# Performance work log

Measured on AMD Instinct MI355X. Metric: run time of the kernel, lower is better.

The kernel has to match this reference:

```python
import jax, jax.numpy as jnp
import numpy as np

N, E, G = 25600, 409600, 128   # nodes, edges, graphs
IN, H, C = 200, 4, 64          # raw feat dim, heads, hidden_channels
IN2 = 2 * IN                   # after NaN-mask concat
BN_EPS = 1e-5

def _glorot(key, shape):
    lim = float(np.sqrt(6.0 / (shape[0] + shape[-1])))
    return jax.random.uniform(key, shape, jnp.float32, -lim, lim)

def setup_inputs():
    key = jax.random.key(0)
    k = iter(jax.random.split(key, 40))
    inp = {
        "x": jax.random.normal(next(k), (N, IN), jnp.float32),
        "edge_index": jax.random.randint(next(k), (2, E), 0, N, jnp.int32),
        "edge_attr": jax.random.normal(next(k), (E, 1), jnp.float32),
        "batch": jnp.repeat(jnp.arange(G, dtype=jnp.int32), N // G),
    }
    dims = [(IN2, H, C), (H * C, H, C), (H * C, 1, C)]
    for i, (din, h, c) in enumerate(dims):
        inp[f"W{i}"] = _glorot(next(k), (din, h * c))
        inp[f"as{i}"] = _glorot(next(k), (h, c))
        inp[f"ad{i}"] = _glorot(next(k), (h, c))
        inp[f"We{i}"] = _glorot(next(k), (1, h * c))
        inp[f"ae{i}"] = _glorot(next(k), (h, c))
        inp[f"b{i}"] = jnp.zeros((h * c,), jnp.float32)
    inp["bn_g"] = jnp.ones((H * C,), jnp.float32)
    inp["bn_b"] = jnp.zeros((H * C,), jnp.float32)
    inp["bn_m"] = jnp.zeros((H * C,), jnp.float32)
    inp["bn_v"] = jnp.ones((H * C,), jnp.float32)
    inp["cw1"] = _glorot(next(k), (C, C))
    inp["cb1"] = jnp.zeros((C,), jnp.float32)
    inp["cw2"] = _glorot(next(k), (C, 2))
    inp["cb2"] = jnp.zeros((2,), jnp.float32)
    return inp

def _gat(x, src, dst, ea, W, att_s, att_d, We, att_e, b, heads, ch):
    """PyG GATConv (edge_dim=1, add_self_loops=True, fill_value='mean', concat=True)."""
    n = x.shape[0]
    # self-loop edge_attr = mean of incoming edge_attr per destination node
    cnt = jax.ops.segment_sum(jnp.ones((ea.shape[0], 1), ea.dtype), dst, n)
    loop_ea = jax.ops.segment_sum(ea, dst, n) / jnp.maximum(cnt, 1.0)
    idx = jnp.arange(n, dtype=src.dtype)
    src = jnp.concatenate([src, idx])
    dst = jnp.concatenate([dst, idx])
    ea = jnp.concatenate([ea, loop_ea], axis=0)
    h = (x @ W).reshape(n, heads, ch)                      # [N,H,C]
    a_s = jnp.einsum('nhc,hc->nh', h, att_s)
    a_d = jnp.einsum('nhc,hc->nh', h, att_d)
    a_e = jnp.einsum('ehc,hc->eh', (ea @ We).reshape(-1, heads, ch), att_e)
    alpha = jax.nn.leaky_relu(a_s[src] + a_d[dst] + a_e, 0.2)   # [E',H]
    # segment softmax over destination neighborhoods
    m = jax.ops.segment_max(alpha, dst, n)
    ex = jnp.exp(alpha - m[dst])
    z = jax.ops.segment_sum(ex, dst, n)
    alpha = ex / (z[dst] + 1e-16)
    out = jax.ops.segment_sum(h[src] * alpha[:, :, None], dst, n)  # [N,H,C]
    return out.reshape(n, heads * ch) + b

def reference(x, edge_index, edge_attr, batch,
              W0, as0, ad0, We0, ae0, b0,
              W1, as1, ad1, We1, ae1, b1,
              W2, as2, ad2, We2, ae2, b2,
              bn_g, bn_b, bn_m, bn_v, cw1, cb1, cw2, cb2):
    nan_mask = jnp.isnan(x).astype(x.dtype)
    x = jnp.concatenate([jnp.nan_to_num(x), nan_mask], axis=-1)   # [N, 2*IN]
    edge_attr = jnp.nan_to_num(edge_attr)
    src, dst = edge_index[0], edge_index[1]
    for (W, a_s, a_d, We, a_e, b) in [(W0, as0, ad0, We0, ae0, b0),
                                      (W1, as1, ad1, We1, ae1, b1)]:
        x = _gat(x, src, dst, edge_attr, W, a_s, a_d, We, a_e, b, H, C)
        x = (x - bn_m) / jnp.sqrt(bn_v + BN_EPS) * bn_g + bn_b    # eval-mode BN
        x = jax.nn.relu(x)                                        # dropout = identity (eval)
    x = _gat(x, src, dst, edge_attr, W2, as2, ad2, We2, ae2, b2, 1, C)
    # global mean pool over graphs
    cnt = jax.ops.segment_sum(jnp.ones((x.shape[0], 1), x.dtype), batch, G)
    g = jax.ops.segment_sum(x, batch, G) / jnp.maximum(cnt, 1.0)  # [G, C]
    hdn = jax.nn.gelu(g @ cw1 + cb1, approximate=False)
    return hdn @ cw2 + cb2                                        # [G, 2]
```

## Files before the change

kernel.cpp:

```cpp
#include <hip/hip_runtime.h>
#include <hip/hip_bf16.h>

static const int kN  = 25600;
static const int kE  = 409600;
static const int kG  = 128;
static const int kNPG = 200;
static const int kIN = 200;
static const int kIN2 = 400;
#define BN_EPS_ 1e-5f

typedef __attribute__((ext_vector_type(8))) short short8;
typedef __attribute__((ext_vector_type(4))) float f32x4;

__device__ __forceinline__ float bu(ushort u) {
  union { float f; unsigned u32; } x; x.u32 = ((unsigned)u) << 16; return x.f;
}
__device__ __forceinline__ ushort f2u(float v) {
  __hip_bfloat16 t = __float2bfloat16(v);
  return *(ushort*)&t;
}
__device__ __forceinline__ float wredSum(float v) {
#pragma unroll
  for (int off = 1; off < 64; off <<= 1) v += __shfl_xor(v, off, 64);
  return v;
}
__device__ __forceinline__ float lrelu(float a) { return (a > 0.f) ? a : 0.2f * a; }

__global__ void k_pre(const float* __restrict__ x, ushort* __restrict__ x2,
                      int* __restrict__ deg,
                      const float* __restrict__ W0, ushort* __restrict__ Wt0,
                      const float* __restrict__ W1, ushort* __restrict__ Wt1,
                      const float* __restrict__ W2, ushort* __restrict__ Wt2,
                      const float* __restrict__ We0, const float* __restrict__ ae0,
                      const float* __restrict__ We1, const float* __restrict__ ae1,
                      const float* __restrict__ We2, const float* __restrict__ ae2,
                      float* __restrict__ wed) {
  int b = blockIdx.x, tid = threadIdx.x;
  if (b < 100) {
    deg[b * 256 + tid] = 0;
    return;
  }
  if (b < 20100) {
    int i = (b - 100) * 256 + tid;
    int n = i / kIN, j = i - n * kIN;
    float v = x[i];
    bool bad = (v != v);
    x2[(size_t)n * kIN2 + j] = f2u(bad ? 0.f : v);
    x2[(size_t)n * kIN2 + kIN + j] = f2u(bad ? 1.f : 0.f);
    return;
  }
  int pb = b - 20100;
  if (pb >= 720) {
    int l = pb - 720;
    const float* We = (l == 0) ? We0 : (l == 1) ? We1 : We2;
    const float* ae = (l == 0) ? ae0 : (l == 1) ? ae1 : ae2;
    int n = (l == 2) ? 64 : 256;
    float v = (tid < n) ? We[tid] * ae[tid] : 0.f;
    v = wredSum(v);
    if ((tid & 63) == 0 && tid < n) wed[l * 4 + (tid >> 6)] = v;
    return;
  }
  int i = pb * 256 + tid;
  if (i < 102400) {
    int n = i / kIN2, k = i - n * kIN2;
    Wt0[(size_t)n * kIN2 + k] = f2u(W0[(size_t)k * 256 + n]);
  } else if (i < 102400 + 65536) {
    int j = i - 102400;
    int n = j >> 8, k = j & 255;
    Wt1[(size_t)n * 256 + k] = f2u(W1[(size_t)k * 256 + n]);
  } else {
    int j = i - 102400 - 65536;
    int n = j >> 8, k = j & 255;
    Wt2[(size_t)n * 256 + k] = f2u(W2[(size_t)k * 64 + n]);
  }
}

#define GBK 64
#define GPAD 72

__global__ __launch_bounds__(256) void k_cnt_gemm0(
    const ushort* __restrict__ A, const ushort* __restrict__ Bt,
    ushort* __restrict__ C, const float* __restrict__ as_g,
    const float* __restrict__ ad_g, float* __restrict__ a_sg,
    float* __restrict__ a_dg, int K,
    const int* __restrict__ ei, int* __restrict__ deg, int* __restrict__ epos) {
  __shared__ ushort As[32 * GPAD];
  __shared__ ushort Bs[256 * GPAD];
  int tid = threadIdx.x;
  if (blockIdx.x >= 800) {
    int e = (blockIdx.x - 800) * 256 + tid;
    if (e < kE) epos[e] = atomicAdd(&deg[ei[kE + e]], 1);
    return;
  }
  int lane = tid & 63, w = tid >> 6;
  int l15 = lane & 15, l4 = lane >> 4;
  int row0 = blockIdx.x * 32;
  f32x4 acc[2][4] = {};
  int ach = tid & 7, arow = tid >> 3;

  for (int kt = 0; kt < K; kt += GBK) {
    __syncthreads();
    {
      int kg = kt + ach * 8;
      short8 v = {0, 0, 0, 0, 0, 0, 0, 0};
      if (kg < K) v = *(const short8*)&A[(size_t)(row0 + arow) * K + kg];
      *(short8*)&As[arow * GPAD + ach * 8] = v;
    }
#pragma unroll
    for (int p = 0; p < 8; p++) {
      int r = p * 32 + arow;
      int kg = kt + ach * 8;
      short8 v = {0, 0, 0, 0, 0, 0, 0, 0};
      if (kg < K) v = *(const short8*)&Bt[(size_t)r * K + kg];
      *(short8*)&Bs[r * GPAD + ach * 8] = v;
    }
    __syncthreads();
#pragma unroll
    for (int kk = 0; kk < 2; kk++) {
      short8 af[2], bf[4];
#pragma unroll
      for (int mi = 0; mi < 2; mi++)
        af[mi] = *(const short8*)&As[(mi * 16 + l15) * GPAD + kk * 32 + l4 * 8];
#pragma unroll
      for (int ni = 0; ni < 4; ni++)
        bf[ni] = *(const short8*)&Bs[(w * 64 + ni * 16 + l15) * GPAD + kk * 32 + l4 * 8];
#pragma unroll
      for (int mi = 0; mi < 2; mi++)
#pragma unroll
        for (int ni = 0; ni < 4; ni++)
          acc[mi][ni] = __builtin_amdgcn_mfma_f32_16x16x32_bf16(af[mi], bf[ni],
                                                                acc[mi][ni], 0, 0, 0);
    }
  }
#pragma unroll
  for (int mi = 0; mi < 2; mi++) {
    int rbase = row0 + mi * 16 + l4 * 4;
#pragma unroll
    for (int ni = 0; ni < 4; ni++) {
      int col = w * 64 + ni * 16 + l15;
#pragma unroll
      for (int r = 0; r < 4; r++)
        C[(size_t)(rbase + r) * 256 + col] = f2u(acc[mi][ni][r]);
    }
  }
  float asv[4], adv[4];
#pragma unroll
  for (int ni = 0; ni < 4; ni++) {
    asv[ni] = as_g[w * 64 + ni * 16 + l15];
    adv[ni] = ad_g[w * 64 + ni * 16 + l15];
  }
#pragma unroll
  for (int mi = 0; mi < 2; mi++) {
#pragma unroll
    for (int r = 0; r < 4; r++) {
      float ps = 0.f, pd = 0.f;
#pragma unroll
      for (int ni = 0; ni < 4; ni++) {
        ps += acc[mi][ni][r] * asv[ni];
        pd += acc[mi][ni][r] * adv[ni];
      }
#pragma unroll
      for (int off = 1; off < 16; off <<= 1) {
        ps += __shfl_xor(ps, off, 64);
        pd += __shfl_xor(pd, off, 64);
      }
      if (l15 == 0) {
        int row = row0 + mi * 16 + l4 * 4 + r;
        a_sg[row * 4 + w] = ps;
        a_dg[row * 4 + w] = pd;
      }
    }
  }
}

__global__ void k_scan_all(const int* __restrict__ deg, int* __restrict__ rowp) {
  __shared__ int s[1024];
  int t = threadIdx.x;
  int base = t * 25;
  int loc[25];
  int sum = 0;
#pragma unroll
  for (int i = 0; i < 25; i++) { loc[i] = sum; sum += deg[base + i]; }
  s[t] = sum;
  __syncthreads();
  for (int off = 1; off < 1024; off <<= 1) {
    int v = (t >= off) ? s[t - off] : 0;
    __syncthreads();
    s[t] += v;
    __syncthreads();
  }
  int excl = s[t] - sum;
#pragma unroll
  for (int i = 0; i < 25; i++) rowp[base + i] = excl + loc[i];
}

__global__ void k_scatter_n(const int* __restrict__ ei, const float* __restrict__ ea,
                            const int* __restrict__ rowp, const int* __restrict__ epos,
                            int* __restrict__ esrc, float* __restrict__ eaC) {
  int e = blockIdx.x * blockDim.x + threadIdx.x;
  if (e >= kE) return;
  int d = ei[kE + e];
  int slot = rowp[d] + d + epos[e];
  esrc[slot] = ei[e];
  float v = ea[e];
  if (v != v) v = 0.f;
  eaC[slot] = v;
}

template <int BN, int MT>
__global__ __launch_bounds__(256) void k_gemm_f(const ushort* __restrict__ A,
                                                const ushort* __restrict__ Bt,
                                                ushort* __restrict__ C,
                                                const float* __restrict__ as_g,
                                                const float* __restrict__ ad_g,
                                                float* __restrict__ a_sg,
                                                float* __restrict__ a_dg, int K) {
  constexpr int MI = (BN == 256) ? (MT / 16) : 1;
  constexpr int H = (BN == 256) ? 4 : 1;
  __shared__ ushort As[MT * GPAD];
  __shared__ ushort Bs[BN * GPAD];
  int tid = threadIdx.x;
  int lane = tid & 63, w = tid >> 6;
  int l15 = lane & 15, l4 = lane >> 4;
  int row0 = blockIdx.y * MT;
  int wr = (BN == 256) ? 0 : (w * 16);
  int wc = (BN == 256) ? (w * 64) : 0;
  f32x4 acc[MI][4] = {};
  int ach = tid & 7, arow = tid >> 3;

  for (int kt = 0; kt < K; kt += GBK) {
    __syncthreads();
#pragma unroll
    for (int p = 0; p < MT / 32; p++) {
      int r = p * 32 + arow;
      int kg = kt + ach * 8;
      short8 v = {0, 0, 0, 0, 0, 0, 0, 0};
      if (kg < K) v = *(const short8*)&A[(size_t)(row0 + r) * K + kg];
      *(short8*)&As[r * GPAD + ach * 8] = v;
    }
#pragma unroll
    for (int p = 0; p < BN / 32; p++) {
      int r = p * 32 + arow;
      int kg = kt + ach * 8;
      short8 v = {0, 0, 0, 0, 0, 0, 0, 0};
      if (kg < K) v = *(const short8*)&Bt[(size_t)r * K + kg];
      *(short8*)&Bs[r * GPAD + ach * 8] = v;
    }
    __syncthreads();
#pragma unroll
    for (int kk = 0; kk < 2; kk++) {
      short8 af[MI], bf[4];
#pragma unroll
      for (int mi = 0; mi < MI; mi++)
        af[mi] = *(const short8*)&As[(wr + mi * 16 + l15) * GPAD + kk * 32 + l4 * 8];
#pragma unroll
      for (int ni = 0; ni < 4; ni++)
        bf[ni] = *(const short8*)&Bs[(wc + ni * 16 + l15) * GPAD + kk * 32 + l4 * 8];
#pragma unroll
      for (int mi = 0; mi < MI; mi++)
#pragma unroll
        for (int ni = 0; ni < 4; ni++)
          acc[mi][ni] = __builtin_amdgcn_mfma_f32_16x16x32_bf16(af[mi], bf[ni],
                                                                acc[mi][ni], 0, 0, 0);
    }
  }
#pragma unroll
  for (int mi = 0; mi < MI; mi++) {
    int rbase = row0 + wr + mi * 16 + l4 * 4;
#pragma unroll
    for (int ni = 0; ni < 4; ni++) {
      int col = wc + ni * 16 + l15;
#pragma unroll
      for (int r = 0; r < 4; r++)
        C[(size_t)(rbase + r) * BN + col] = f2u(acc[mi][ni][r]);
    }
  }
  float asv[4], adv[4];
#pragma unroll
  for (int ni = 0; ni < 4; ni++) {
    asv[ni] = as_g[wc + ni * 16 + l15];
    adv[ni] = ad_g[wc + ni * 16 + l15];
  }
  int hh = (BN == 256) ? w : 0;
#pragma unroll
  for (int mi = 0; mi < MI; mi++) {
#pragma unroll
    for (int r = 0; r < 4; r++) {
      float ps = 0.f, pd = 0.f;
#pragma unroll
      for (int ni = 0; ni < 4; ni++) {
        ps += acc[mi][ni][r] * asv[ni];
        pd += acc[mi][ni][r] * adv[ni];
      }
#pragma unroll
      for (int off = 1; off < 16; off <<= 1) {
        ps += __shfl_xor(ps, off, 64);
        pd += __shfl_xor(pd, off, 64);
      }
      if (l15 == 0) {
        int row = row0 + wr + mi * 16 + l4 * 4 + r;
        a_sg[row * H + hh] = ps;
        a_dg[row * H + hh] = pd;
      }
    }
  }
}

__global__ __launch_bounds__(256) void k_agg4(
    const ushort* __restrict__ hbuf, const int* __restrict__ rowp,
    const int* __restrict__ deg, const int* __restrict__ esrc,
    const float* __restrict__ eaC, const float* __restrict__ a_s,
    const float* __restrict__ a_d, const float* __restrict__ wed,
    const float* __restrict__ bias, const float* __restrict__ bng,
    const float* __restrict__ bnb, const float* __restrict__ bnm,
    const float* __restrict__ bnv, ushort* __restrict__ xout) {
  int tid = threadIdx.x;
  int w = tid >> 6, lane = tid & 63;
  int d = blockIdx.x * 4 + w;
  int start = rowp[d] + d;
  int dg = deg[d];
  int h = lane >> 4;
  float adh = a_d[d * 4 + h];
  float wdh = wed[h];

  int c0 = lane * 4;
  float a0 = 0.f, a1 = 0.f, a2 = 0.f, a3 = 0.f, sz = 0.f, sea = 0.f;
  int k = 0;
  for (; k + 4 <= dg; k += 4) {
    int s0 = esrc[start + k], s1 = esrc[start + k + 1];
    int s2 = esrc[start + k + 2], s3 = esrc[start + k + 3];
    float e0 = eaC[start + k], e1 = eaC[start + k + 1];
    float e2 = eaC[start + k + 2], e3 = eaC[start + k + 3];
    ushort4 v0 = *(const ushort4*)&hbuf[(size_t)s0 * 256 + c0];
    ushort4 v1 = *(const ushort4*)&hbuf[(size_t)s1 * 256 + c0];
    ushort4 v2 = *(const ushort4*)&hbuf[(size_t)s2 * 256 + c0];
    ushort4 v3 = *(const ushort4*)&hbuf[(size_t)s3 * 256 + c0];
    float w0 = __expf(lrelu(a_s[s0 * 4 + h] + adh + e0 * wdh));
    float w1 = __expf(lrelu(a_s[s1 * 4 + h] + adh + e1 * wdh));
    float w2 = __expf(lrelu(a_s[s2 * 4 + h] + adh + e2 * wdh));
    float w3 = __expf(lrelu(a_s[s3 * 4 + h] + adh + e3 * wdh));
    sea += (e0 + e1) + (e2 + e3);
    sz += (w0 + w1) + (w2 + w3);
    a0 += w0 * bu(v0.x) + w1 * bu(v1.x) + w2 * bu(v2.x) + w3 * bu(v3.x);
    a1 += w0 * bu(v0.y) + w1 * bu(v1.y) + w2 * bu(v2.y) + w3 * bu(v3.y);
    a2 += w0 * bu(v0.z) + w1 * bu(v1.z) + w2 * bu(v2.z) + w3 * bu(v3.z);
    a3 += w0 * bu(v0.w) + w1 * bu(v1.w) + w2 * bu(v2.w) + w3 * bu(v3.w);
  }
  for (; k < dg; k++) {
    int s0 = esrc[start + k];
    float e0 = eaC[start + k];
    ushort4 v0 = *(const ushort4*)&hbuf[(size_t)s0 * 256 + c0];
    float w0 = __expf(lrelu(a_s[s0 * 4 + h] + adh + e0 * wdh));
    sea += e0;
    sz += w0;
    a0 += w0 * bu(v0.x); a1 += w0 * bu(v0.y);
    a2 += w0 * bu(v0.z); a3 += w0 * bu(v0.w);
  }
  {
    float lea = sea / fmaxf((float)dg, 1.f);
    ushort4 v0 = *(const ushort4*)&hbuf[(size_t)d * 256 + c0];
    float w0 = __expf(lrelu(a_s[d * 4 + h] + adh + lea * wdh));
    sz += w0;
    a0 += w0 * bu(v0.x); a1 += w0 * bu(v0.y);
    a2 += w0 * bu(v0.z); a3 += w0 * bu(v0.w);
  }
  float winv = 1.f / (sz + 1e-16f);

  float4 bi = *(const float4*)&bias[c0];
  a0 = a0 * winv + bi.x; a1 = a1 * winv + bi.y;
  a2 = a2 * winv + bi.z; a3 = a3 * winv + bi.w;
  float4 g4 = *(const float4*)&bng[c0], b4 = *(const float4*)&bnb[c0];
  float4 m4 = *(const float4*)&bnm[c0], v4 = *(const float4*)&bnv[c0];
  a0 = fmaxf((a0 - m4.x) * rsqrtf(v4.x + BN_EPS_) * g4.x + b4.x, 0.f);
  a1 = fmaxf((a1 - m4.y) * rsqrtf(v4.y + BN_EPS_) * g4.y + b4.y, 0.f);
  a2 = fmaxf((a2 - m4.z) * rsqrtf(v4.z + BN_EPS_) * g4.z + b4.z, 0.f);
  a3 = fmaxf((a3 - m4.w) * rsqrtf(v4.w + BN_EPS_) * g4.w + b4.w, 0.f);
  ushort4 o = make_ushort4(f2u(a0), f2u(a1), f2u(a2), f2u(a3));
  *(ushort4*)&xout[(size_t)d * 256 + c0] = o;
}

__global__ __launch_bounds__(256) void k_agg1(
    const ushort* __restrict__ hbuf, const int* __restrict__ rowp,
    const int* __restrict__ deg, const int* __restrict__ esrc,
    const float* __restrict__ eaC, const float* __restrict__ a_s,
    const float* __restrict__ a_d, const float* __restrict__ wed,
    const float* __restrict__ bias, float* __restrict__ xout) {
  int tid = threadIdx.x;
  int w = tid >> 6, lane = tid & 63;
  int d = blockIdx.x * 4 + w;
  int start = rowp[d] + d;
  int dg = deg[d];
  float adh = a_d[d];
  float wdh = wed[0];

  float acc = 0.f, sz = 0.f, sea = 0.f;
  int k = 0;
  for (; k + 4 <= dg; k += 4) {
    int s0 = esrc[start + k], s1 = esrc[start + k + 1];
    int s2 = esrc[start + k + 2], s3 = esrc[start + k + 3];
    float e0 = eaC[start + k], e1 = eaC[start + k + 1];
    float e2 = eaC[start + k + 2], e3 = eaC[start + k + 3];
    float v0 = bu(hbuf[(size_t)s0 * 64 + lane]);
    float v1 = bu(hbuf[(size_t)s1 * 64 + lane]);
    float v2 = bu(hbuf[(size_t)s2 * 64 + lane]);
    float v3 = bu(hbuf[(size_t)s3 * 64 + lane]);
    float w0 = __expf(lrelu(a_s[s0] + adh + e0 * wdh));
    float w1 = __expf(lrelu(a_s[s1] + adh + e1 * wdh));
    float w2 = __expf(lrelu(a_s[s2] + adh + e2 * wdh));
    float w3 = __expf(lrelu(a_s[s3] + adh + e3 * wdh));
    sea += (e0 + e1) + (e2 + e3);
    sz += (w0 + w1) + (w2 + w3);
    acc += w0 * v0 + w1 * v1 + w2 * v2 + w3 * v3;
  }
  for (; k < dg; k++) {
    int s0 = esrc[start + k];
    float e0 = eaC[start + k];
    float w0 = __expf(lrelu(a_s[s0] + adh + e0 * wdh));
    sea += e0;
    sz += w0;
    acc += w0 * bu(hbuf[(size_t)s0 * 64 + lane]);
  }
  {
    float lea = sea / fmaxf((float)dg, 1.f);
    float w0 = __expf(lrelu(a_s[d] + adh + lea * wdh));
    sz += w0;
    acc += w0 * bu(hbuf[(size_t)d * 64 + lane]);
  }
  acc = acc / (sz + 1e-16f) + bias[lane];
  xout[(size_t)d * 64 + lane] = acc;
}

__global__ void k_poolhead(const float* __restrict__ xin,
                           const float* __restrict__ cw1, const float* __restrict__ cb1,
                           const float* __restrict__ cw2, const float* __restrict__ cb2,
                           float* __restrict__ out) {
  __shared__ float part[4][64];
  __shared__ float gb[64], hb[64];
  int g = blockIdx.x, tid = threadIdx.x;
  int c = tid & 63, w = tid >> 6;
  float acc = 0.f;
  size_t base = (size_t)g * kNPG * 64;
  for (int n = w; n < kNPG; n += 4) acc += xin[base + (size_t)n * 64 + c];
  part[w][c] = acc;
  __syncthreads();
  if (tid < 64) {
    float s = (part[0][c] + part[1][c]) + (part[2][c] + part[3][c]);
    gb[c] = s * (1.f / kNPG);
  }
  __syncthreads();
  if (tid < 64) {
    float s = cb1[c];
#pragma unroll 8
    for (int i = 0; i < 64; i++) s += gb[i] * cw1[i * 64 + c];
    s = 0.5f * s * (1.f + erff(s * 0.70710678118654752f));
    hb[c] = s;
  }
  __syncthreads();
  if (tid < 2) {
    float o = cb2[tid];
    for (int i = 0; i < 64; i++) o += hb[i] * cw2[i * 2 + tid];
    out[g * 2 + tid] = o;
  }
}


extern "C" void kernel_launch(void* const* d_in, const int* in_sizes, int n_in,
                              void* d_out, int out_size, void* d_ws, size_t ws_size,
                              hipStream_t stream) {
  (void)in_sizes; (void)n_in; (void)out_size; (void)ws_size;
  const float* x  = (const float*)d_in[0];
  const int* ei   = (const int*)d_in[1];
  const float* ea = (const float*)d_in[2];
  const float *W[3], *as_[3], *ad_[3], *We[3], *ae[3], *bi[3];
  for (int l = 0; l < 3; l++) {
    W[l]   = (const float*)d_in[4 + l * 6 + 0];
    as_[l] = (const float*)d_in[4 + l * 6 + 1];
    ad_[l] = (const float*)d_in[4 + l * 6 + 2];
    We[l]  = (const float*)d_in[4 + l * 6 + 3];
    ae[l]  = (const float*)d_in[4 + l * 6 + 4];
    bi[l]  = (const float*)d_in[4 + l * 6 + 5];
  }
  const float* bng = (const float*)d_in[22];
  const float* bnb = (const float*)d_in[23];
  const float* bnm = (const float*)d_in[24];
  const float* bnv = (const float*)d_in[25];
  const float* cw1 = (const float*)d_in[26];
  const float* cb1 = (const float*)d_in[27];
  const float* cw2 = (const float*)d_in[28];
  const float* cb2 = (const float*)d_in[29];

  char* p = (char*)d_ws;
  auto alloc = [&](size_t bytes) -> void* {
    void* r = (void*)p;
    p += (bytes + 255) & ~(size_t)255;
    return r;
  };
  ushort* x2b   = (ushort*)alloc((size_t)kN * kIN2 * 2);
  ushort* hbufb = (ushort*)alloc((size_t)kN * 256 * 2);
  ushort* xbA   = (ushort*)alloc((size_t)kN * 256 * 2);
  ushort* xbB   = (ushort*)alloc((size_t)kN * 256 * 2);
  float*  fbuf  = (float*)alloc((size_t)kN * 64 * 4);
  ushort* Wt0   = (ushort*)alloc((size_t)kIN2 * 256 * 2);
  ushort* Wt1   = (ushort*)alloc((size_t)256 * 256 * 2);
  ushort* Wt2   = (ushort*)alloc((size_t)256 * 64 * 2);
  float* a_s    = (float*)alloc((size_t)kN * 4 * 4);
  float* a_d    = (float*)alloc((size_t)kN * 4 * 4);
  int* rowp     = (int*)alloc((size_t)kN * 4);
  int* esrc     = (int*)alloc((size_t)(kE + kN) * 4);
  float* eaC    = (float*)alloc((size_t)(kE + kN) * 4);
  int* epos     = (int*)alloc((size_t)kE * 4);
  float* wed    = (float*)alloc(256);
  int* deg      = (int*)alloc((size_t)kN * 4);

  k_pre<<<100 + 20000 + 723, 256, 0, stream>>>(x, x2b, deg, W[0], Wt0, W[1], Wt1,
                                               W[2], Wt2, We[0], ae[0], We[1], ae[1],
                                               We[2], ae[2], wed);
  k_cnt_gemm0<<<2400, 256, 0, stream>>>(x2b, Wt0, hbufb, as_[0], ad_[0],
                                        a_s, a_d, kIN2, ei, deg, epos);
  k_scan_all<<<1, 1024, 0, stream>>>(deg, rowp);
  k_scatter_n<<<(kE + 255) / 256, 256, 0, stream>>>(ei, ea, rowp, epos, esrc, eaC);
  k_agg4<<<kN / 4, 256, 0, stream>>>(hbufb, rowp, deg, esrc, eaC, a_s, a_d,
                                     &wed[0], bi[0], bng, bnb, bnm, bnv, xbA);
  dim3 gg32(1, kN / 32);
  k_gemm_f<256, 32><<<gg32, 256, 0, stream>>>(xbA, Wt1, hbufb, as_[1], ad_[1],
                                              a_s, a_d, 256);
  k_agg4<<<kN / 4, 256, 0, stream>>>(hbufb, rowp, deg, esrc, eaC, a_s, a_d,
                                     &wed[4], bi[1], bng, bnb, bnm, bnv, xbB);
  dim3 gg64(1, kN / 64);
  k_gemm_f<64, 64><<<gg64, 256, 0, stream>>>(xbB, Wt2, hbufb, as_[2], ad_[2],
                                             a_s, a_d, 256);
  k_agg1<<<kN / 4, 256, 0, stream>>>(hbufb, rowp, deg, esrc, eaC, a_s, a_d,
                                     &wed[8], bi[2], fbuf);
  k_poolhead<<<kG, 256, 0, stream>>>(fbuf, cw1, cb1, cw2, cb2, (float*)d_out);
}
```

Before: 339.0 us.

## Replace global atomic degree counting with per-block LDS histograms and column scan

Edge degree counting moves from global atomics, previously fused into the first GEMM kernel, to 64 blocks. Each block builds a per-block LDS histogram over all nodes, and a column-wise prefix scan across blocks turns those into per-block offsets. The scatter then adds each edge's block offset to its local position. The first GEMM now runs through the generic k_gemm_f kernel, and the deg zeroing in k_pre is dropped. This removes contended global atomics but adds a 6.5MB blockcnt buffer plus two extra launches, and the histogram blocks may see low occupancy because each uses 100KB of LDS.

After: 332.2 us. 1.02x faster.

```diff
diff --git a/kernel.cpp b/kernel.cpp
--- a/kernel.cpp
+++ b/kernel.cpp
@@ -7,6 +7,8 @@
 static const int kNPG = 200;
 static const int kIN = 200;
 static const int kIN2 = 400;
+static const int kHB = 64;
+static const int kEPB = kE / kHB;
 #define BN_EPS_ 1e-5f
 
 typedef __attribute__((ext_vector_type(8))) short short8;
@@ -27,7 +29,6 @@
 __device__ __forceinline__ float lrelu(float a) { return (a > 0.f) ? a : 0.2f * a; }
 
 __global__ void k_pre(const float* __restrict__ x, ushort* __restrict__ x2,
-                      int* __restrict__ deg,
                       const float* __restrict__ W0, ushort* __restrict__ Wt0,
                       const float* __restrict__ W1, ushort* __restrict__ Wt1,
                       const float* __restrict__ W2, ushort* __restrict__ Wt2,
@@ -36,12 +37,8 @@
                       const float* __restrict__ We2, const float* __restrict__ ae2,
                       float* __restrict__ wed) {
   int b = blockIdx.x, tid = threadIdx.x;
-  if (b < 100) {
-    deg[b * 256 + tid] = 0;
-    return;
-  }
-  if (b < 20100) {
-    int i = (b - 100) * 256 + tid;
+  if (b < 20000) {
+    int i = b * 256 + tid;
     int n = i / kIN, j = i - n * kIN;
     float v = x[i];
     bool bad = (v != v);
@@ -49,7 +46,7 @@
     x2[(size_t)n * kIN2 + kIN + j] = f2u(bad ? 1.f : 0.f);
     return;
   }
-  int pb = b - 20100;
+  int pb = b - 20000;
   if (pb >= 720) {
     int l = pb - 720;
     const float* We = (l == 0) ? We0 : (l == 1) ? We1 : We2;
@@ -75,102 +72,34 @@
   }
 }
 
-#define GBK 64
-#define GPAD 72
-
-__global__ __launch_bounds__(256) void k_cnt_gemm0(
-    const ushort* __restrict__ A, const ushort* __restrict__ Bt,
-    ushort* __restrict__ C, const float* __restrict__ as_g,
-    const float* __restrict__ ad_g, float* __restrict__ a_sg,
-    float* __restrict__ a_dg, int K,
-    const int* __restrict__ ei, int* __restrict__ deg, int* __restrict__ epos) {
-  __shared__ ushort As[32 * GPAD];
-  __shared__ ushort Bs[256 * GPAD];
-  int tid = threadIdx.x;
-  if (blockIdx.x >= 800) {
-    int e = (blockIdx.x - 800) * 256 + tid;
-    if (e < kE) epos[e] = atomicAdd(&deg[ei[kE + e]], 1);
-    return;
-  }
-  int lane = tid & 63, w = tid >> 6;
-  int l15 = lane & 15, l4 = lane >> 4;
-  int row0 = blockIdx.x * 32;
-  f32x4 acc[2][4] = {};
-  int ach = tid & 7, arow = tid >> 3;
-
-  for (int kt = 0; kt < K; kt += GBK) {
-    __syncthreads();
-    {
-      int kg = kt + ach * 8;
-      short8 v = {0, 0, 0, 0, 0, 0, 0, 0};
-      if (kg < K) v = *(const short8*)&A[(size_t)(row0 + arow) * K + kg];
-      *(short8*)&As[arow * GPAD + ach * 8] = v;
-    }
-#pragma unroll
-    for (int p = 0; p < 8; p++) {
-      int r = p * 32 + arow;
-      int kg = kt + ach * 8;
-      short8 v = {0, 0, 0, 0, 0, 0, 0, 0};
-      if (kg < K) v = *(const short8*)&Bt[(size_t)r * K + kg];
-      *(short8*)&Bs[r * GPAD + ach * 8] = v;
-    }
-    __syncthreads();
-#pragma unroll
-    for (int kk = 0; kk < 2; kk++) {
-      short8 af[2], bf[4];
-#pragma unroll
-      for (int mi = 0; mi < 2; mi++)
-        af[mi] = *(const short8*)&As[(mi * 16 + l15) * GPAD + kk * 32 + l4 * 8];
-#pragma unroll
-      for (int ni = 0; ni < 4; ni++)
-        bf[ni] = *(const short8*)&Bs[(w * 64 + ni * 16 + l15) * GPAD + kk * 32 + l4 * 8];
-#pragma unroll
-      for (int mi = 0; mi < 2; mi++)
-#pragma unroll
-        for (int ni = 0; ni < 4; ni++)
-          acc[mi][ni] = __builtin_amdgcn_mfma_f32_16x16x32_bf16(af[mi], bf[ni],
-                                                                acc[mi][ni], 0, 0, 0);
-    }
-  }
-#pragma unroll
-  for (int mi = 0; mi < 2; mi++) {
-    int rbase = row0 + mi * 16 + l4 * 4;
-#pragma unroll
-    for (int ni = 0; ni < 4; ni++) {
-      int col = w * 64 + ni * 16 + l15;
-#pragma unroll
-      for (int r = 0; r < 4; r++)
-        C[(size_t)(rbase + r) * 256 + col] = f2u(acc[mi][ni][r]);
-    }
-  }
-  float asv[4], adv[4];
-#pragma unroll
-  for (int ni = 0; ni < 4; ni++) {
-    asv[ni] = as_g[w * 64 + ni * 16 + l15];
-    adv[ni] = ad_g[w * 64 + ni * 16 + l15];
-  }
-#pragma unroll
-  for (int mi = 0; mi < 2; mi++) {
-#pragma unroll
-    for (int r = 0; r < 4; r++) {
-      float ps = 0.f, pd = 0.f;
-#pragma unroll
-      for (int ni = 0; ni < 4; ni++) {
-        ps += acc[mi][ni][r] * asv[ni];
-        pd += acc[mi][ni][r] * adv[ni];
-      }
-#pragma unroll
-      for (int off = 1; off < 16; off <<= 1) {
-        ps += __shfl_xor(ps, off, 64);
-        pd += __shfl_xor(pd, off, 64);
-      }
-      if (l15 == 0) {
-        int row = row0 + mi * 16 + l4 * 4 + r;
-        a_sg[row * 4 + w] = ps;
-        a_dg[row * 4 + w] = pd;
-      }
-    }
-  }
+__global__ __launch_bounds__(1024) void k_hist(const int* __restrict__ ei,
+                                               int* __restrict__ epos,
+                                               int* __restrict__ blockcnt) {
+  __shared__ int cnt[kN];
+  int t = threadIdx.x, b = blockIdx.x;
+  for (int i = t; i < kN; i += 1024) cnt[i] = 0;
+  __syncthreads();
+  int base = b * kEPB;
+  for (int i = t; i < kEPB; i += 1024) {
+    int e = base + i;
+    int d = ei[kE + e];
+    epos[e] = atomicAdd(&cnt[d], 1);
+  }
+  __syncthreads();
+  for (int i = t; i < kN; i += 1024) blockcnt[(size_t)b * kN + i] = cnt[i];
+}
+
+__global__ void k_colscan(int* __restrict__ blockcnt, int* __restrict__ deg) {
+  int n = blockIdx.x * 256 + threadIdx.x;
+  int acc = 0;
+#pragma unroll 8
+  for (int b = 0; b < kHB; b++) {
+    size_t idx = (size_t)b * kN + n;
+    int v = blockcnt[idx];
+    blockcnt[idx] = acc;
+    acc += v;
+  }
+  deg[n] = acc;
 }
 
 __global__ void k_scan_all(const int* __restrict__ deg, int* __restrict__ rowp) {
@@ -196,16 +125,21 @@
 
 __global__ void k_scatter_n(const int* __restrict__ ei, const float* __restrict__ ea,
                             const int* __restrict__ rowp, const int* __restrict__ epos,
+                            const int* __restrict__ blockcnt,
                             int* __restrict__ esrc, float* __restrict__ eaC) {
   int e = blockIdx.x * blockDim.x + threadIdx.x;
   if (e >= kE) return;
   int d = ei[kE + e];
-  int slot = rowp[d] + d + epos[e];
+  int b = e / kEPB;
+  int slot = rowp[d] + d + blockcnt[(size_t)b * kN + d] + epos[e];
   esrc[slot] = ei[e];
   float v = ea[e];
   if (v != v) v = 0.f;
   eaC[slot] = v;
 }
+
+#define GBK 64
+#define GPAD 72
 
 template <int BN, int MT>
 __global__ __launch_bounds__(256) void k_gemm_f(const ushort* __restrict__ A,
@@ -509,19 +443,23 @@
   int* esrc     = (int*)alloc((size_t)(kE + kN) * 4);
   float* eaC    = (float*)alloc((size_t)(kE + kN) * 4);
   int* epos     = (int*)alloc((size_t)kE * 4);
+  int* blockcnt = (int*)alloc((size_t)kHB * kN * 4);
   float* wed    = (float*)alloc(256);
   int* deg      = (int*)alloc((size_t)kN * 4);
 
-  k_pre<<<100 + 20000 + 723, 256, 0, stream>>>(x, x2b, deg, W[0], Wt0, W[1], Wt1,
-                                               W[2], Wt2, We[0], ae[0], We[1], ae[1],
-                                               We[2], ae[2], wed);
-  k_cnt_gemm0<<<2400, 256, 0, stream>>>(x2b, Wt0, hbufb, as_[0], ad_[0],
-                                        a_s, a_d, kIN2, ei, deg, epos);
+  k_pre<<<20000 + 720 + 3, 256, 0, stream>>>(x, x2b, W[0], Wt0, W[1], Wt1,
+                                             W[2], Wt2, We[0], ae[0], We[1], ae[1],
+                                             We[2], ae[2], wed);
+  k_hist<<<kHB, 1024, 0, stream>>>(ei, epos, blockcnt);
+  k_colscan<<<kN / 256, 256, 0, stream>>>(blockcnt, deg);
   k_scan_all<<<1, 1024, 0, stream>>>(deg, rowp);
-  k_scatter_n<<<(kE + 255) / 256, 256, 0, stream>>>(ei, ea, rowp, epos, esrc, eaC);
+  k_scatter_n<<<(kE + 255) / 256, 256, 0, stream>>>(ei, ea, rowp, epos, blockcnt,
+                                                    esrc, eaC);
+  dim3 gg32(1, kN / 32);
+  k_gemm_f<256, 32><<<gg32, 256, 0, stream>>>(x2b, Wt0, hbufb, as_[0], ad_[0],
+                                              a_s, a_d, kIN2);
   k_agg4<<<kN / 4, 256, 0, stream>>>(hbufb, rowp, deg, esrc, eaC, a_s, a_d,
                                      &wed[0], bi[0], bng, bnb, bnm, bnv, xbA);
-  dim3 gg32(1, kN / 32);
   k_gemm_f<256, 32><<<gg32, 256, 0, stream>>>(xbA, Wt1, hbufb, as_[1], ad_[1],
                                               a_s, a_d, 256);
   k_agg4<<<kN / 4, 256, 0, stream>>>(hbufb, rowp, deg, esrc, eaC, a_s, a_d,
```
